# Kernel optimization log

Measured on AMD Instinct MI355X. Metric: run time of the kernel, lower is better.

## Reference

```python
import jax, jax.numpy as jnp
import numpy as np

N_HEADS = 16
HEAD_DIM = 64
WINDOW = 128
GLOBAL = 64


def setup_inputs() -> dict:
    key = jax.random.key(0)
    ks = jax.random.split(key, 5)
    B, T, D = 2, 8192, 1024
    s = 0.02
    return {
        "x": jax.random.normal(ks[0], (B, T, D), dtype=jnp.float32),
        "Wq": jax.random.normal(ks[1], (D, D), dtype=jnp.float32) * s,
        "Wk": jax.random.normal(ks[2], (D, D), dtype=jnp.float32) * s,
        "Wv": jax.random.normal(ks[3], (D, D), dtype=jnp.float32) * s,
        "Wo": jax.random.normal(ks[4], (D, D), dtype=jnp.float32) * s,
    }


def reference(x, Wq, Wk, Wv, Wo):
    B, T, D = x.shape
    h, hd, w = N_HEADS, HEAD_DIM, WINDOW
    g = min(GLOBAL, T)
    nw = T // w  # T chosen as a multiple of window_size
    scale = hd ** -0.5

    def proj(W):
        # nn.Linear: y = x @ W.T ; then (B,T,h,hd) -> (B,h,T,hd)
        return (x @ W.T).reshape(B, T, h, hd).transpose(0, 2, 1, 3)

    q = proj(Wq)
    k = proj(Wk)
    v = proj(Wv)

    # Chunk into non-overlapping local windows: (B,h,nw,w,hd)
    qw = q.reshape(B, h, nw, w, hd)
    kw = k.reshape(B, h, nw, w, hd)
    vw = v.reshape(B, h, nw, w, hd)
    kg = k[:, :, :g, :]  # global prefix keys (B,h,g,hd)
    vg = v[:, :, :g, :]

    # Scores against [global ++ local] keys (faithful: global prefix is
    # concatenated for every window, including windows that overlap it).
    s_g = jnp.einsum("bhnqd,bhgd->bhnqg", qw, kg) * scale  # (B,h,nw,w,g)
    s_l = jnp.einsum("bhnqd,bhnkd->bhnqk", qw, kw) * scale  # (B,h,nw,w,w)
    attn = jax.nn.softmax(jnp.concatenate([s_g, s_l], axis=-1), axis=-1)

    out = (
        jnp.einsum("bhnqg,bhgd->bhnqd", attn[..., :g], vg)
        + jnp.einsum("bhnqk,bhnkd->bhnqd", attn[..., g:], vw)
    )
    out = out.reshape(B, h, T, hd).transpose(0, 2, 1, 3).reshape(B, T, D)
    return out @ Wo.T
```

## Files before the change

kernel.cpp:

```cpp
#include <hip/hip_runtime.h>

typedef unsigned short u16;
typedef __attribute__((ext_vector_type(8))) short short8;
typedef __attribute__((ext_vector_type(4))) float f32x4;
typedef __attribute__((ext_vector_type(4))) float floatx4;
typedef __attribute__((ext_vector_type(4))) unsigned short ushort4v;
typedef __attribute__((ext_vector_type(8))) unsigned short ushort8v;

#define MFMA(a, b, c)   __builtin_amdgcn_mfma_f32_16x16x32_bf16(a, b, c, 0, 0, 0)

__device__ __forceinline__ u16 f2bf(float f) {
    unsigned u = __float_as_uint(f);
    u += 0x7fffu + ((u >> 16) & 1u);
    return (u16)(u >> 16);
}

__device__ __forceinline__ void async16(const void* g, void* l) {
    __builtin_amdgcn_global_load_lds(
        (const __attribute__((address_space(1))) void*)g,
        (__attribute__((address_space(3))) void*)l, 16, 0, 0);
}

#define SYNC(n) do {                                             \
    asm volatile("s_waitcnt vmcnt(" #n ")" ::: "memory");        \
    __builtin_amdgcn_s_barrier();                                \
    asm volatile("" ::: "memory");                               \
    __builtin_amdgcn_sched_barrier(0);                           \
} while (0)

__global__ void cvt_all(const float* __restrict__ x,
                        const float* __restrict__ w0, const float* __restrict__ w1,
                        const float* __restrict__ w2, const float* __restrict__ w3,
                        u16* __restrict__ d, int nx4, int nw4) {
    int total = nx4 + 4 * nw4;
    int i = blockIdx.x * blockDim.x + threadIdx.x;
    int stride = gridDim.x * blockDim.x;
    for (; i < total; i += stride) {
        floatx4 v;
        if (i < nx4) {
            v = ((const floatx4*)x)[i];
        } else {
            int t = i - nx4;
            int w = t >> 18;
            int j = t & (nw4 - 1);
            const float* s = w == 0 ? w0 : (w == 1 ? w1 : (w == 2 ? w2 : w3));
            v = ((const floatx4*)s)[j];
        }
        ushort4v o;
        o[0] = f2bf(v[0]); o[1] = f2bf(v[1]); o[2] = f2bf(v[2]); o[3] = f2bf(v[3]);
        ((ushort4v*)d)[i] = o;
    }
}

template <bool BF16_OUT>
__global__ __launch_bounds__(512, 2) void gemm_nt(
    const u16* __restrict__ A, const u16* __restrict__ B0,
    const u16* __restrict__ B1, const u16* __restrict__ B2,
    void* __restrict__ Cv, int M, int N, int K)
{
    __shared__ u16 As[2][16384];
    __shared__ u16 Bs[2][16384];
    const int tid = threadIdx.x;
    const int wave = tid >> 6, lane = tid & 63;
    const int tl = lane & 15, quad = lane >> 4, xr = lane & 7;
    const int wm = wave >> 2, wn = wave & 3;
    const int m0 = blockIdx.x * 256, n0 = blockIdx.y * 256;
    const u16* Bm = blockIdx.z == 0 ? B0 : (blockIdx.z == 1 ? B1 : B2);
    const size_t coff = (size_t)blockIdx.z * M * N;

    f32x4 acc[8][4];
#pragma unroll
    for (int i = 0; i < 8; i++)
#pragma unroll
        for (int j = 0; j < 4; j++) acc[i][j] = (f32x4)(0.0f);

    const int rw = lane >> 3, sl = lane & 7;
    const int g = sl ^ rw;
    const u16* a_srcb = A  + (size_t)(m0 + wave * 8 + rw) * K + g * 8;
    const u16* b_srcb = Bm + (size_t)(n0 + (wave >> 2) * 64 + (wave & 3) * 8 + rw) * K + g * 8;
    u16* asd = &As[0][0] + wave * 512;
    u16* bsd = &Bs[0][0] + (wave >> 2) * 4096 + (wave & 3) * 512;

#define STG_A(t, h, p) do {                                                              \
    async16(a_srcb + (size_t)((h) * 64) * K + (size_t)(t) * 64,                          \
            asd + (p) * 16384 + (h) * 4096);                                             \
    async16(a_srcb + (size_t)((h) * 64 + 128) * K + (size_t)(t) * 64,                    \
            asd + (p) * 16384 + (h) * 4096 + 8192);                                      \
} while (0)
#define STG_B(t, h, p) do {                                                              \
    async16(b_srcb + (size_t)((h) * 32) * K + (size_t)(t) * 64,                          \
            bsd + (p) * 16384 + (h) * 2048);                                             \
    async16(b_srcb + (size_t)((h) * 32 + 128) * K + (size_t)(t) * 64,                    \
            bsd + (p) * 16384 + (h) * 2048 + 8192);                                      \
} while (0)

    const int NT = K >> 6;
    const u16* Ab0 = &As[0][0] + (wm * 128 + tl) * 64;
    const u16* Bb0 = &Bs[0][0] + (wn * 64 + tl) * 64;
    const int s0 = (quad ^ xr) * 8;

    short8 afA[4][2], afB[4][2], bfA[2][2], bfB[2][2];

    STG_A(0, 0, 0); STG_B(0, 0, 0); STG_A(0, 1, 0); STG_B(0, 1, 0);

    for (int t = 0; t < NT; ++t) {
        const int p = t & 1, pq = p ^ 1;
        const bool pf = (t + 1) < NT;
        const u16* Ab = Ab0 + p * 16384;
        const u16* Bb = Bb0 + p * 16384;

        SYNC(4);
#pragma unroll
        for (int i = 0; i < 4; i++) {
            afA[i][0] = *(const short8*)(Ab + i * 1024 + s0);
            afA[i][1] = *(const short8*)(Ab + i * 1024 + (s0 ^ 32));
        }
#pragma unroll
        for (int j = 0; j < 2; j++) {
            bfA[j][0] = *(const short8*)(Bb + j * 1024 + s0);
            bfA[j][1] = *(const short8*)(Bb + j * 1024 + (s0 ^ 32));
        }
        if (pf) STG_A(t + 1, 0, pq);
        __builtin_amdgcn_s_setprio(1);
#pragma unroll
        for (int kh = 0; kh < 2; kh++)
#pragma unroll
            for (int i = 0; i < 4; i++)
#pragma unroll
                for (int j = 0; j < 2; j++)
                    acc[i][j] = MFMA(afA[i][kh], bfA[j][kh], acc[i][j]);
        __builtin_amdgcn_s_setprio(0);

        if (pf) { SYNC(4); } else { SYNC(2); }
#pragma unroll
        for (int i = 0; i < 4; i++) {
            afB[i][0] = *(const short8*)(Ab + (4 + i) * 1024 + s0);
            afB[i][1] = *(const short8*)(Ab + (4 + i) * 1024 + (s0 ^ 32));
        }
        if (pf) STG_B(t + 1, 0, pq);
        __builtin_amdgcn_s_setprio(1);
#pragma unroll
        for (int kh = 0; kh < 2; kh++)
#pragma unroll
            for (int i = 0; i < 4; i++)
#pragma unroll
                for (int j = 0; j < 2; j++)
                    acc[4 + i][j] = MFMA(afB[i][kh], bfA[j][kh], acc[4 + i][j]);
        __builtin_amdgcn_s_setprio(0);

        if (pf) { SYNC(4); } else { SYNC(0); }
#pragma unroll
        for (int j = 0; j < 2; j++) {
            bfB[j][0] = *(const short8*)(Bb + (2 + j) * 1024 + s0);
            bfB[j][1] = *(const short8*)(Bb + (2 + j) * 1024 + (s0 ^ 32));
        }
        if (pf) STG_A(t + 1, 1, pq);
        __builtin_amdgcn_s_setprio(1);
#pragma unroll
        for (int kh = 0; kh < 2; kh++)
#pragma unroll
            for (int i = 0; i < 4; i++)
#pragma unroll
                for (int j = 0; j < 2; j++)
                    acc[4 + i][2 + j] = MFMA(afB[i][kh], bfB[j][kh], acc[4 + i][2 + j]);
        __builtin_amdgcn_s_setprio(0);

        if (pf) STG_B(t + 1, 1, pq);
        __builtin_amdgcn_s_setprio(1);
#pragma unroll
        for (int kh = 0; kh < 2; kh++)
#pragma unroll
            for (int i = 0; i < 4; i++)
#pragma unroll
                for (int j = 0; j < 2; j++)
                    acc[i][2 + j] = MFMA(afA[i][kh], bfB[j][kh], acc[i][2 + j]);
        __builtin_amdgcn_s_setprio(0);
    }
#undef STG_A
#undef STG_B

#pragma unroll
    for (int mf = 0; mf < 8; mf++)
#pragma unroll
        for (int nf = 0; nf < 4; nf++)
#pragma unroll
            for (int r = 0; r < 4; r++) {
                int row = m0 + wm * 128 + mf * 16 + quad * 4 + r;
                int col = n0 + wn * 64 + nf * 16 + tl;
                if constexpr (BF16_OUT)
                    ((u16*)Cv)[coff + (size_t)row * N + col] = f2bf(acc[mf][nf][r]);
                else
                    ((float*)Cv)[coff + (size_t)row * N + col] = acc[mf][nf][r];
            }
}

__global__ __launch_bounds__(512, 4) void attn_win(
    const u16* __restrict__ qkv, u16* __restrict__ outb)
{
    constexpr int T = 8192, D = 1024, HD = 64, G = 64, WIN = 128;
    constexpr int MTOT = 2 * T;
    __shared__ u16 Vs[192 * 64];
    __shared__ u16 Ks[192 * 64];
    __shared__ u16 Vt[64 * 200];

    const int blk = blockIdx.x;
    const int nwin = blk & 63;
    const int h = (blk >> 6) & 15;
    const int b = blk >> 10;
    const int tid = threadIdx.x;
    const int wave = tid >> 6, lane = tid & 63;
    const int quad = lane >> 4, tl = lane & 15;
    const int win0 = nwin * WIN;
    const size_t brow = (size_t)b * T;
    const u16* qb = qkv;
    const u16* kb = qkv + (size_t)MTOT * D;
    const u16* vb = qkv + (size_t)2 * MTOT * D;

    short8 bq[2];
    {
        int tok = win0 + wave * 16 + tl;
        const u16* qrow = qb + (brow + tok) * D + h * HD;
        bq[0] = *(const short8*)(qrow + quad * 8);
        bq[1] = *(const short8*)(qrow + 32 + quad * 8);
    }
    __builtin_amdgcn_sched_barrier(0);

#pragma unroll
    for (int i = 0; i < 3; i++) {
        int ch = i * 512 + tid;
        int row = ch >> 3, c = ch & 7;
        int tok = row < G ? row : win0 + (row - G);
        async16(vb + (brow + tok) * D + h * HD + c * 8,
                Vs + (i * 512 + wave * 64) * 8);
    }
#pragma unroll
    for (int i = 0; i < 3; i++) {
        int ch = i * 512 + tid;
        int row = ch >> 3, slot = ch & 7;
        int gg = slot ^ (row & 7);
        int tok = row < G ? row : win0 + (row - G);
        async16(kb + (brow + tok) * D + h * HD + gg * 8,
                Ks + (i * 512 + wave * 64) * 8);
    }

    asm volatile("s_waitcnt vmcnt(3)" ::: "memory");
    __builtin_amdgcn_s_barrier();
    __builtin_amdgcn_sched_barrier(0);

    {
        const int d = lane;
#pragma unroll
        for (int i = 0; i < 3; i++) {
            int c = wave * 3 + i;
            ushort8v v;
#pragma unroll
            for (int j = 0; j < 8; j++) v[j] = Vs[(c * 8 + j) * 64 + d];
            *(ushort8v*)&Vt[d * 200 + c * 8] = v;
        }
    }

    asm volatile("s_waitcnt vmcnt(0) lgkmcnt(0)" ::: "memory");
    __builtin_amdgcn_s_barrier();
    __builtin_amdgcn_sched_barrier(0);

    f32x4 s[12];
#pragma unroll
    for (int kt = 0; kt < 12; kt++) s[kt] = (f32x4)(0.0f);
#pragma unroll
    for (int kt = 0; kt < 12; kt++) {
        int row = kt * 16 + tl;
        int sa = quad ^ (tl & 7);
        int sb = (4 + quad) ^ (tl & 7);
        short8 a0 = *(const short8*)&Ks[row * 64 + sa * 8];
        short8 a1 = *(const short8*)&Ks[row * 64 + sb * 8];
        s[kt] = MFMA(a0, bq[0], s[kt]);
        s[kt] = MFMA(a1, bq[1], s[kt]);
    }

    const float c1 = 0.125f * 1.4426950408889634f;
    float mx = -1e30f;
#pragma unroll
    for (int kt = 0; kt < 12; kt++)
#pragma unroll
        for (int r = 0; r < 4; r++) mx = fmaxf(mx, s[kt][r]);
    mx = fmaxf(mx, __shfl_xor(mx, 16, 64));
    mx = fmaxf(mx, __shfl_xor(mx, 32, 64));
    float sum = 0.f;
#pragma unroll
    for (int kt = 0; kt < 12; kt++)
#pragma unroll
        for (int r = 0; r < 4; r++) {
            float e = exp2f((s[kt][r] - mx) * c1);
            s[kt][r] = e;
            sum += e;
        }
    sum += __shfl_xor(sum, 16, 64);
    sum += __shfl_xor(sum, 32, 64);
    float inv = 1.f / sum;

    __syncthreads();

    const int lq = wave * 16 + tl;
    u16* Pr = (lq < 64) ? (Vs + lq * 192) : (Ks + (lq - 64) * 192);
#pragma unroll
    for (int kt = 0; kt < 12; kt++) {
        ushort4v pk;
#pragma unroll
        for (int r = 0; r < 4; r++) pk[r] = f2bf(s[kt][r] * inv);
        *(ushort4v*)&Pr[((((kt * 2) + (quad >> 1)) ^ (lq & 7)) << 3) + ((quad & 1) << 2)] = pk;
    }
    __syncthreads();

    f32x4 o[4];
#pragma unroll
    for (int dt = 0; dt < 4; dt++) o[dt] = (f32x4)(0.0f);
#pragma unroll
    for (int ks = 0; ks < 6; ks++) {
        short8 pa = *(const short8*)&Pr[(((ks * 4) + quad) ^ (lq & 7)) << 3];
#pragma unroll
        for (int dt = 0; dt < 4; dt++) {
            short8 vv = *(const short8*)&Vt[(dt * 16 + tl) * 200 + ks * 32 + quad * 8];
            o[dt] = MFMA(pa, vv, o[dt]);
        }
    }

#pragma unroll
    for (int dt = 0; dt < 4; dt++)
#pragma unroll
        for (int r = 0; r < 4; r++) {
            int qq = win0 + wave * 16 + quad * 4 + r;
            int dim = dt * 16 + tl;
            outb[(brow + qq) * D + h * HD + dim] = f2bf(o[dt][r]);
        }
}

extern "C" void kernel_launch(void* const* d_in, const int* in_sizes, int n_in,
                              void* d_out, int out_size, void* d_ws, size_t ws_size,
                              hipStream_t stream)
{
    const float* x  = (const float*)d_in[0];
    const float* Wq = (const float*)d_in[1];
    const float* Wk = (const float*)d_in[2];
    const float* Wv = (const float*)d_in[3];
    const float* Wo = (const float*)d_in[4];

    const int M = 16384, D = 1024;
    u16* xb  = (u16*)d_ws;
    u16* wqb = xb  + (size_t)M * D;
    u16* wob = wqb + (size_t)3 * D * D;
    u16* qkv = wob + (size_t)D * D;
    u16* att = qkv + (size_t)3 * M * D;

    cvt_all<<<2560, 256, 0, stream>>>(x, Wq, Wk, Wv, Wo, xb,
                                      M * D / 4, D * D / 4);

    gemm_nt<true ><<<dim3(M / 256, D / 256, 3), 512, 0, stream>>>(
        xb, wqb, wqb + (size_t)D * D, wqb + (size_t)2 * D * D, qkv, M, D, D);
    attn_win<<<dim3(2048), 512, 0, stream>>>(qkv, att);
    gemm_nt<false><<<dim3(M / 256, D / 256, 1), 512, 0, stream>>>(
        att, wob, wob, wob, d_out, M, D, D);
}
```

Before: 303.9 us.

## Use 128x128-tile 32x32 MFMA GEMM for output projection and drop a barrier

Adds a new GEMM kernel with 128x128 tiles, 256 threads and 32x32x16 bf16 MFMAs, and uses it for the final output projection in place of the 256x256-tile kernel. The smaller tiles give 1024 blocks instead of 256, which should fill the CUs better on this skinny N=1024 problem. The new kernel has no double buffering, and its load, barrier, compute sequence may expose memory latency. The change also removes the __syncthreads between writing P to LDS and reading it back in the attention kernel. Each wave reads only the P rows it wrote itself, so removing the barrier is likely safe.

Result: slower. 314.9 us (+3.6%).

```diff
diff --git a/kernel.cpp b/kernel.cpp
--- a/kernel.cpp
+++ b/kernel.cpp
@@ -3,11 +3,13 @@
 typedef unsigned short u16;
 typedef __attribute__((ext_vector_type(8))) short short8;
 typedef __attribute__((ext_vector_type(4))) float f32x4;
+typedef __attribute__((ext_vector_type(16))) float f32x16;
 typedef __attribute__((ext_vector_type(4))) float floatx4;
 typedef __attribute__((ext_vector_type(4))) unsigned short ushort4v;
 typedef __attribute__((ext_vector_type(8))) unsigned short ushort8v;
 
 #define MFMA(a, b, c)   __builtin_amdgcn_mfma_f32_16x16x32_bf16(a, b, c, 0, 0, 0)
+#define MFMA32(a, b, c) __builtin_amdgcn_mfma_f32_32x32x16_bf16(a, b, c, 0, 0, 0)
 
 __device__ __forceinline__ u16 f2bf(float f) {
     unsigned u = __float_as_uint(f);
@@ -194,6 +196,81 @@
             }
 }
 
+template <bool BF16_OUT>
+__global__ __launch_bounds__(256) void gemm_nt128(
+    const u16* __restrict__ A, const u16* __restrict__ B0,
+    const u16* __restrict__ B1, const u16* __restrict__ B2,
+    void* __restrict__ Cv, int M, int N, int K)
+{
+    __shared__ u16 As[128 * 64];
+    __shared__ u16 Bs[128 * 64];
+    const int tid = threadIdx.x;
+    const int wave = tid >> 6, lane = tid & 63;
+    const int l32 = lane & 31, kh = lane >> 5;
+    const int m0 = blockIdx.x * 128, n0 = blockIdx.y * 128;
+    const int wm = wave >> 1, wn = wave & 1;
+    const u16* Bm = blockIdx.z == 0 ? B0 : (blockIdx.z == 1 ? B1 : B2);
+    const size_t coff = (size_t)blockIdx.z * M * N;
+
+    f32x16 acc[2][2];
+#pragma unroll
+    for (int i = 0; i < 2; i++)
+#pragma unroll
+        for (int j = 0; j < 2; j++) acc[i][j] = (f32x16)(0.0f);
+
+    const int srow = tid >> 3, sslot = tid & 7;
+    const int gch = sslot ^ (srow & 7);
+    const u16* ar[4];
+    const u16* br[4];
+#pragma unroll
+    for (int i = 0; i < 4; i++) {
+        ar[i] = A  + (size_t)(m0 + i * 32 + srow) * K + gch * 8;
+        br[i] = Bm + (size_t)(n0 + i * 32 + srow) * K + gch * 8;
+    }
+
+    const int rxor = l32 & 7;
+
+    for (int k0 = 0; k0 < K; k0 += 64) {
+#pragma unroll
+        for (int i = 0; i < 4; i++) {
+            int ldsbase = (i * 256 + wave * 64) * 8;
+            async16(ar[i] + k0, (u16*)As + ldsbase);
+            async16(br[i] + k0, (u16*)Bs + ldsbase);
+        }
+        __syncthreads();
+#pragma unroll
+        for (int kc = 0; kc < 4; kc++) {
+            const int rs = ((kc * 2 + kh) ^ rxor) * 8;
+            short8 af[2], bg[2];
+#pragma unroll
+            for (int t = 0; t < 2; t++) {
+                af[t] = *(const short8*)&As[(wm * 64 + t * 32 + l32) * 64 + rs];
+                bg[t] = *(const short8*)&Bs[(wn * 64 + t * 32 + l32) * 64 + rs];
+            }
+#pragma unroll
+            for (int mt = 0; mt < 2; mt++)
+#pragma unroll
+                for (int nt = 0; nt < 2; nt++)
+                    acc[mt][nt] = MFMA32(af[mt], bg[nt], acc[mt][nt]);
+        }
+        __syncthreads();
+    }
+
+#pragma unroll
+    for (int mt = 0; mt < 2; mt++)
+#pragma unroll
+        for (int nt = 0; nt < 2; nt++)
+#pragma unroll
+            for (int r = 0; r < 16; r++) {
+                int row = m0 + wm * 64 + mt * 32 + 4 * kh + (r & 3) + 8 * (r >> 2);
+                int col = n0 + wn * 64 + nt * 32 + l32;
+                if constexpr (BF16_OUT)
+                    ((u16*)Cv)[coff + (size_t)row * N + col] = f2bf(acc[mt][nt][r]);
+                else
+                    ((float*)Cv)[coff + (size_t)row * N + col] = acc[mt][nt][r];
+            }
+}
+
 __global__ __launch_bounds__(512, 4) void attn_win(
     const u16* __restrict__ qkv, u16* __restrict__ outb)
 {
@@ -309,7 +386,6 @@
         for (int r = 0; r < 4; r++) pk[r] = f2bf(s[kt][r] * inv);
         *(ushort4v*)&Pr[((((kt * 2) + (quad >> 1)) ^ (lq & 7)) << 3) + ((quad & 1) << 2)] = pk;
     }
-    __syncthreads();
 
     f32x4 o[4];
 #pragma unroll
@@ -357,6 +433,6 @@
     gemm_nt<true ><<<dim3(M / 256, D / 256, 3), 512, 0, stream>>>(
         xb, wqb, wqb + (size_t)D * D, wqb + (size_t)2 * D * D, qkv, M, D, D);
     attn_win<<<dim3(2048), 512, 0, stream>>>(qkv, att);
-    gemm_nt<false><<<dim3(M / 256, D / 256, 1), 512, 0, stream>>>(
+    gemm_nt128<false><<<dim3(M / 128, D / 128, 1), 256, 0, stream>>>(
         att, wob, wob, wob, d_out, M, D, D);
 }
```
